# Kernel tuning notes

Measured on AMD Instinct MI355X. Metric: run time of the kernel, lower is better.

The kernel has to match this reference:

```python
import jax, jax.numpy as jnp
import numpy as np

EPS_LN = 1e-5


def fwht(x):
    """Fast Walsh-Hadamard transform over the last axis (power-of-two length).
    Vectorized butterfly: log2(n) stages, each a reshape + add/sub."""
    orig_shape = x.shape
    n = orig_shape[-1]
    y = x.reshape(-1, n)
    h = 1
    while h < n:
        y = y.reshape(-1, n // (2 * h), 2, h)
        a = y[:, :, 0, :]
        b = y[:, :, 1, :]
        y = jnp.stack([a + b, a - b], axis=2).reshape(-1, n)
        h <<= 1
    return y.reshape(orig_shape)


def setup_inputs() -> dict:
    key = jax.random.key(0)
    kx, kw, kg = jax.random.split(key, 3)
    B, S, D_IN, D_OUT = 4, 4096, 2048, 2048
    x = jax.random.normal(kx, (B, S, D_IN), dtype=jnp.float32)
    # kaiming_uniform_(a=sqrt(5)) -> bound = 1/sqrt(in_features)
    bound = 1.0 / np.sqrt(D_IN)
    W = jax.random.uniform(kw, (D_OUT, D_IN), dtype=jnp.float32,
                           minval=-bound, maxval=bound)
    gamma = jnp.ones((D_IN,), dtype=jnp.float32)
    beta = jnp.zeros((D_IN,), dtype=jnp.float32)
    return {"x": x, "W": W, "gamma": gamma, "beta": beta}


def reference(x, W, gamma, beta):
    bits = 4
    max_val = (1 << (bits - 1)) - 1  # 7
    # LayerNorm over last dim
    mu = jnp.mean(x, axis=-1, keepdims=True)
    var = jnp.mean(jnp.square(x - mu), axis=-1, keepdims=True)
    x_ln = (x - mu) * jax.lax.rsqrt(var + EPS_LN) * gamma + beta
    # Activation fake-quant to `bits` bits (per-row absmax scale)
    x_scale = jnp.clip(jnp.max(jnp.abs(x_ln), axis=-1, keepdims=True), 1e-6, None)
    x_int = jnp.clip(jnp.round(x_ln * max_val / x_scale), -max_val, max_val)
    x_q = x_int * x_scale / max_val
    # Hadamard transform of quantized activations
    x_h = fwht(x_q)
    # Ternary weight quantization with global mean-abs scale
    w_scale = jnp.clip(jnp.mean(jnp.abs(W)), 1e-6, None)
    w_q = (jnp.where(W > 0.5 * w_scale, 1.0, 0.0)
           + jnp.where(W < -0.5 * w_scale, -1.0, 0.0)) * w_scale
    # Linear (no bias), then second Hadamard transform
    out = jnp.einsum('bsd,od->bso', x_h, w_q)
    return fwht(out)
```

## Files before the change

kernel.cpp:

```cpp
#include <hip/hip_runtime.h>

typedef unsigned short u16;
typedef __attribute__((ext_vector_type(8))) __bf16 bf16x8;
typedef __attribute__((ext_vector_type(4))) float floatx4;

#define DDIM 2048
#define MROWS 16384

__device__ __forceinline__ u16 f2bf(float f) {
    unsigned int u = __builtin_bit_cast(unsigned int, f);
    u = (u + 0x7fffu + ((u >> 16) & 1u)) >> 16;
    return (u16)u;
}

__device__ __forceinline__ float wave_sum(float v) {
#pragma unroll
    for (int o = 32; o > 0; o >>= 1) v += __shfl_down(v, o, 64);
    return v;
}
__device__ __forceinline__ float wave_max(float v) {
#pragma unroll
    for (int o = 32; o > 0; o >>= 1) v = fmaxf(v, __shfl_down(v, o, 64));
    return v;
}

__global__ __launch_bounds__(256) void absmean_part(const float4* __restrict__ W4,
                                                    float* __restrict__ partial) {
    float s = 0.f;
    for (int i = blockIdx.x * 256 + threadIdx.x; i < (DDIM * DDIM / 4); i += 1024 * 256) {
        float4 v = W4[i];
        s += fabsf(v.x) + fabsf(v.y) + fabsf(v.z) + fabsf(v.w);
    }
    s = wave_sum(s);
    __shared__ float red[4];
    if ((threadIdx.x & 63) == 0) red[threadIdx.x >> 6] = s;
    __syncthreads();
    if (threadIdx.x == 0) partial[blockIdx.x] = red[0] + red[1] + red[2] + red[3];
}

#define CFP 9

template <bool QUANT, bool BF16OUT>
__global__ __launch_bounds__(256) void colfwht(const float* __restrict__ in,
                                               void* __restrict__ out,
                                               const float* __restrict__ partial) {
    extern __shared__ float S[];
    const int t = threadIdx.x;
    const int c8 = blockIdx.x * 8;

    float wsc = 0.f, half_t = 0.f;
    if (QUANT) {
        __shared__ float wred[4];
        float s = partial[t] + partial[t + 256] + partial[t + 512] + partial[t + 768];
        s = wave_sum(s);
        if ((t & 63) == 0) wred[t >> 6] = s;
        __syncthreads();
        float m = (wred[0] + wred[1] + wred[2] + wred[3]) * (1.0f / (float)(DDIM * DDIM));
        wsc = fmaxf(m, 1e-6f);
        half_t = 0.5f * wsc;
    }

#pragma unroll
    for (int i = 0; i < 16; ++i) {
        const int k = i * 256 + t;
        const int row = k >> 1, half = k & 1;
        float4 v = *(const float4*)(in + (size_t)row * DDIM + c8 + half * 4);
        if (QUANT) {
            v.x = (v.x > half_t ? wsc : 0.f) + (v.x < -half_t ? -wsc : 0.f);
            v.y = (v.y > half_t ? wsc : 0.f) + (v.y < -half_t ? -wsc : 0.f);
            v.z = (v.z > half_t ? wsc : 0.f) + (v.z < -half_t ? -wsc : 0.f);
            v.w = (v.w > half_t ? wsc : 0.f) + (v.w < -half_t ? -wsc : 0.f);
        }
        float* sp = S + row * CFP + half * 4;
        sp[0] = v.x; sp[1] = v.y; sp[2] = v.z; sp[3] = v.w;
    }
    __syncthreads();

#pragma unroll
    for (int s = 0; s < 5; ++s) {
        const int h = 1 << (2 * s);
#pragma unroll
        for (int i = 0; i < 16; ++i) {
            const int task = i * 256 + t;
            const int p = task >> 3, c = task & 7;
            const int i0 = ((p >> (2 * s)) << (2 * s + 2)) | (p & (h - 1));
            float* a0 = S + (size_t)i0 * CFP + c;
            const float x0 = a0[0];
            const float x1 = a0[(size_t)h * CFP];
            const float x2 = a0[(size_t)2 * h * CFP];
            const float x3 = a0[(size_t)3 * h * CFP];
            const float s01 = x0 + x1, d01 = x0 - x1;
            const float s23 = x2 + x3, d23 = x2 - x3;
            a0[0]                   = s01 + s23;
            a0[(size_t)h * CFP]     = d01 + d23;
            a0[(size_t)2 * h * CFP] = s01 - s23;
            a0[(size_t)3 * h * CFP] = d01 - d23;
        }
        __syncthreads();
    }
#pragma unroll
    for (int i = 0; i < 32; ++i) {
        const int task = i * 256 + t;
        const int p = task >> 3, c = task & 7;
        float* a0 = S + (size_t)p * CFP + c;
        const float x0 = a0[0];
        const float x1 = a0[(size_t)1024 * CFP];
        a0[0] = x0 + x1;
        a0[(size_t)1024 * CFP] = x0 - x1;
    }
    __syncthreads();

    const int c = t >> 5, l = t & 31;
#pragma unroll
    for (int i = 0; i < 16; ++i) {
        const int o4 = i * 32 + l;
        const float r0 = S[(size_t)(o4 * 4 + 0) * CFP + c];
        const float r1 = S[(size_t)(o4 * 4 + 1) * CFP + c];
        const float r2 = S[(size_t)(o4 * 4 + 2) * CFP + c];
        const float r3 = S[(size_t)(o4 * 4 + 3) * CFP + c];
        if (BF16OUT) {
            uint2 v;
            v.x = (unsigned)f2bf(r0) | ((unsigned)f2bf(r1) << 16);
            v.y = (unsigned)f2bf(r2) | ((unsigned)f2bf(r3) << 16);
            ((uint2*)((u16*)out + (size_t)(c8 + c) * DDIM))[o4] = v;
        } else {
            ((float4*)((float*)out + (size_t)(c8 + c) * DDIM))[o4] =
                make_float4(r0, r1, r2, r3);
        }
    }
}

__global__ __launch_bounds__(256) void ln_quant(const float* __restrict__ X,
                                                const float* __restrict__ G,
                                                const float* __restrict__ Bt,
                                                u16* __restrict__ XQ) {
    const int row = blockIdx.x;
    const int t = threadIdx.x;
    const float4* rp = (const float4*)(X + (size_t)row * DDIM);
    float4 v0 = rp[t], v1 = rp[t + 256];
    float v[8] = {v0.x, v0.y, v0.z, v0.w, v1.x, v1.y, v1.z, v1.w};

    __shared__ float redA[4], redB[4], redC[4];
    const int wv = t >> 6, ln = t & 63;

    float s = 0.f, s2 = 0.f;
#pragma unroll
    for (int j = 0; j < 8; ++j) { s += v[j]; s2 += v[j] * v[j]; }
#pragma unroll
    for (int o = 32; o > 0; o >>= 1) {
        s += __shfl_down(s, o, 64);
        s2 += __shfl_down(s2, o, 64);
    }
    if (ln == 0) { redA[wv] = s; redB[wv] = s2; }
    __syncthreads();
    const float mu = (redA[0] + redA[1] + redA[2] + redA[3]) * (1.f / (float)DDIM);
    const float ex2 = (redB[0] + redB[1] + redB[2] + redB[3]) * (1.f / (float)DDIM);
    const float var = ex2 - mu * mu;
    const float rstd = rsqrtf(var + 1e-5f);

    const float4* gp = (const float4*)G;
    const float4* bp = (const float4*)Bt;
    float4 g0 = gp[t], g1 = gp[t + 256];
    float4 b0 = bp[t], b1 = bp[t + 256];
    float gg[8] = {g0.x, g0.y, g0.z, g0.w, g1.x, g1.y, g1.z, g1.w};
    float bb[8] = {b0.x, b0.y, b0.z, b0.w, b1.x, b1.y, b1.z, b1.w};

    float y[8];
    float am = 0.f;
#pragma unroll
    for (int j = 0; j < 8; ++j) {
        y[j] = (v[j] - mu) * rstd * gg[j] + bb[j];
        am = fmaxf(am, fabsf(y[j]));
    }
    float w = wave_max(am);
    if (ln == 0) redC[wv] = w;
    __syncthreads();
    const float scale = fmaxf(fmaxf(fmaxf(redC[0], redC[1]), fmaxf(redC[2], redC[3])), 1e-6f);

    const float r7 = 7.f / scale, s7 = scale / 7.f;
    unsigned int q[4];
#pragma unroll
    for (int j = 0; j < 8; j += 2) {
        float qa = fminf(fmaxf(rintf(y[j] * r7), -7.f), 7.f);
        float qb = fminf(fmaxf(rintf(y[j + 1] * r7), -7.f), 7.f);
        q[j >> 1] = (unsigned)f2bf(qa * s7) | ((unsigned)f2bf(qb * s7) << 16);
    }
    uint2 o0, o1;
    o0.x = q[0]; o0.y = q[1]; o1.x = q[2]; o1.y = q[3];
    uint2* orow = (uint2*)(XQ + (size_t)row * DDIM);
    orow[t] = o0;
    orow[t + 256] = o1;
}

#define GBK 64
#define GNT (DDIM / GBK)
#define NITER (GNT / 2)
#define TILEU (256 * GBK)

__device__ __forceinline__ void gl_lds16(const u16* g, u16* l) {
    __builtin_amdgcn_global_load_lds((const __attribute__((address_space(1))) void*)g,
                                     (__attribute__((address_space(3))) void*)l,
                                     16, 0, 0);
}

#define PBAR do {                                                              \
    __builtin_amdgcn_sched_barrier(0);                                         \
    asm volatile("" ::: "memory");                                             \
    __builtin_amdgcn_s_barrier();                                              \
    asm volatile("" ::: "memory");                                             \
    __builtin_amdgcn_sched_barrier(0);                                         \
} while (0)

#define PWAIT8 do {                                                            \
    __builtin_amdgcn_sched_barrier(0);                                         \
    asm volatile("s_waitcnt vmcnt(8)" ::: "memory");                           \
    __builtin_amdgcn_s_barrier();                                              \
    asm volatile("" ::: "memory");                                             \
    __builtin_amdgcn_sched_barrier(0);                                         \
} while (0)

#define PWAIT0 do {                                                            \
    __builtin_amdgcn_sched_barrier(0);                                         \
    asm volatile("s_waitcnt vmcnt(0)" ::: "memory");                           \
    __builtin_amdgcn_s_barrier();                                              \
    asm volatile("" ::: "memory");                                             \
    __builtin_amdgcn_sched_barrier(0);                                         \
} while (0)

__global__ __launch_bounds__(512, 2) void gemm256(const u16* __restrict__ A,
                                                  const u16* __restrict__ B,
                                                  float* __restrict__ C) {
    extern __shared__ __align__(16) u16 lds[];
    const int t = threadIdx.x;
    const int lane = t & 63;
    const int wid = t >> 6;
    const int wm = wid >> 2;
    const int wn = wid & 3;

    const int d = blockIdx.x;
    const int bm = (d & 7) | ((d >> 6) << 3);
    const int bn = (d >> 3) & 7;

    const int l15 = lane & 15;
    const int kq = lane >> 4;
    const int x7 = lane & 7;
    const int c0 = (kq ^ x7) << 3;
    const int c1 = ((kq | 4) ^ x7) << 3;
    const int arow = (wm << 7) + l15;
    const int brow = (wn << 6) + l15;

    const int srow = t >> 3;
    const int gch = ((t & 7) ^ (srow & 7)) << 3;
    const u16* Ag = A + (size_t)(bm * 256 + srow) * DDIM + gch;
    const u16* Bg = B + (size_t)(bn * 256 + srow) * DDIM + gch;
    u16* const AL0 = lds + t * 8;
    u16* const BL0 = lds + TILEU + t * 8;
    u16* const AL1 = lds + 2 * TILEU + t * 8;
    u16* const BL1 = lds + 3 * TILEU + t * 8;
    const u16* const Ab0 = lds;
    const u16* const Bb0 = lds + TILEU;
    const u16* const Ab1 = lds + 2 * TILEU;
    const u16* const Bb1 = lds + 3 * TILEU;

    floatx4 acc[8][4];
#pragma unroll
    for (int i = 0; i < 8; ++i)
#pragma unroll
        for (int j = 0; j < 4; ++j)
#pragma unroll
            for (int e = 0; e < 4; ++e) acc[i][j][e] = 0.f;

    bf16x8 a[4][2], b0v[2][2], b1v[2][2];

#define STGA(dst, q, ko) gl_lds16(Ag + (size_t)((q) * 64) * DDIM + (ko), (dst) + (q) * 4096)
#define STGB(dst, q, ko) gl_lds16(Bg + (size_t)((q) * 64) * DDIM + (ko), (dst) + (q) * 4096)

#define LDA(Ab, mh)                                                            \
    _Pragma("unroll") for (int fm = 0; fm < 4; ++fm) {                         \
        const u16* p = (Ab) + (arow + (mh) * 64 + fm * 16) * GBK;              \
        a[fm][0] = *(const bf16x8*)(p + c0);                                   \
        a[fm][1] = *(const bf16x8*)(p + c1);                                   \
    }

#define LDB(dst, Bb, nh)                                                       \
    _Pragma("unroll") for (int fn = 0; fn < 2; ++fn) {                         \
        const u16* p = (Bb) + (brow + (nh) * 32 + fn * 16) * GBK;              \
        dst[fn][0] = *(const bf16x8*)(p + c0);                                 \
        dst[fn][1] = *(const bf16x8*)(p + c1);                                 \
    }

#define MMA(mh, bsrc, nh)                                                      \
    __builtin_amdgcn_s_setprio(1);                                             \
    _Pragma("unroll") for (int fm = 0; fm < 4; ++fm)                           \
        _Pragma("unroll") for (int fn = 0; fn < 2; ++fn)                       \
            _Pragma("unroll") for (int ks = 0; ks < 2; ++ks)                   \
                acc[(mh) * 4 + fm][(nh) * 2 + fn] =                            \
                    __builtin_amdgcn_mfma_f32_16x16x32_bf16(                   \
                        a[fm][ks], bsrc[fn][ks],                               \
                        acc[(mh) * 4 + fm][(nh) * 2 + fn], 0, 0, 0);           \
    __builtin_amdgcn_s_setprio(0);

#pragma unroll
    for (int q = 0; q < 4; ++q) STGA(AL0, q, 0);
#pragma unroll
    for (int q = 0; q < 4; ++q) STGB(BL0, q, 0);
#pragma unroll
    for (int q = 0; q < 4; ++q) STGA(AL1, q, GBK);
#pragma unroll
    for (int q = 0; q < 4; ++q) STGB(BL1, q, GBK);
    PWAIT8;

    for (int it = 0; it < NITER; ++it) {
        const int kp0 = (it * 2 + 2) * GBK;
        const int kp1 = kp0 + GBK;
        const bool pf = (it < NITER - 1);

        LDA(Ab0, 0);
        LDB(b0v, Bb0, 0);
        PBAR;
        MMA(0, b0v, 0);
        LDB(b1v, Bb0, 1);
        if (pf) { STGA(AL0, 0, kp0); STGA(AL0, 2, kp0); }
        PBAR;
        MMA(0, b1v, 1);
        LDA(Ab0, 1);
        if (pf) { STGB(BL0, 0, kp0); STGB(BL0, 1, kp0); }
        PBAR;
        MMA(1, b0v, 0);
        if (pf) { STGB(BL0, 2, kp0); STGB(BL0, 3, kp0); STGA(AL0, 1, kp0); STGA(AL0, 3, kp0); }
        if (pf) { PWAIT8; } else { PWAIT0; }
        MMA(1, b1v, 1);

        LDA(Ab1, 0);
        LDB(b0v, Bb1, 0);
        PBAR;
        MMA(0, b0v, 0);
        LDB(b1v, Bb1, 1);
        if (pf) { STGA(AL1, 0, kp1); STGA(AL1, 2, kp1); }
        PBAR;
        MMA(0, b1v, 1);
        LDA(Ab1, 1);
        if (pf) { STGB(BL1, 0, kp1); STGB(BL1, 1, kp1); }
        PBAR;
        MMA(1, b0v, 0);
        if (pf) { STGB(BL1, 2, kp1); STGB(BL1, 3, kp1); STGA(AL1, 1, kp1); STGA(AL1, 3, kp1); }
        if (pf) { PWAIT8; } else { PWAIT0; }
        MMA(1, b1v, 1);
    }

#undef STGA
#undef STGB
#undef LDA
#undef LDB
#undef MMA

    float* Cb = C + (size_t)(bm * 256 + (wm << 7) + (lane >> 4) * 4) * DDIM
                  + bn * 256 + (wn << 6) + l15;
#pragma unroll
    for (int fm = 0; fm < 8; ++fm)
#pragma unroll
        for (int fn = 0; fn < 4; ++fn)
#pragma unroll
            for (int r = 0; r < 4; ++r)
                Cb[(size_t)(fm * 16 + r) * DDIM + fn * 16] = acc[fm][fn][r];
}

extern "C" void kernel_launch(void* const* d_in, const int* in_sizes, int n_in,
                              void* d_out, int out_size, void* d_ws, size_t ws_size,
                              hipStream_t stream) {
    const float* X  = (const float*)d_in[0];
    const float* W  = (const float*)d_in[1];
    const float* G  = (const float*)d_in[2];
    const float* Bt = (const float*)d_in[3];
    float* out = (float*)d_out;

    char* ws = (char*)d_ws;
    u16*   xq   = (u16*)ws;
    float* bufA = (float*)(ws + (size_t)67108864);
    float* bufB = (float*)(ws + (size_t)67108864 + 16777216);
    float* partial = bufB;
    u16*   w3      = (u16*)bufB;

    absmean_part<<<1024, 256, 0, stream>>>((const float4*)W, partial);

    {
        void (*k1)(const float*, void*, const float*) = colfwht<true, false>;
        void (*k2)(const float*, void*, const float*) = colfwht<false, true>;
        hipFuncSetAttribute(reinterpret_cast<const void*>(k1),
                            hipFuncAttributeMaxDynamicSharedMemorySize, DDIM * CFP * 4);
        hipFuncSetAttribute(reinterpret_cast<const void*>(k2),
                            hipFuncAttributeMaxDynamicSharedMemorySize, DDIM * CFP * 4);
        colfwht<true, false><<<256, 256, DDIM * CFP * 4, stream>>>(W, (void*)bufA, partial);
        colfwht<false, true><<<256, 256, DDIM * CFP * 4, stream>>>(bufA, (void*)w3, nullptr);
    }

    ln_quant<<<MROWS, 256, 0, stream>>>(X, G, Bt, xq);

    hipFuncSetAttribute(reinterpret_cast<const void*>(gemm256),
                        hipFuncAttributeMaxDynamicSharedMemorySize, 131072);
    gemm256<<<dim3(512), 512, 131072, stream>>>(xq, w3, out);
}
```

Measured before the change: 386.9 us.

## Fuse weight column-FWHT passes with LayerNorm quantization into shared launches

```diff
diff --git a/kernel.cpp b/kernel.cpp
--- a/kernel.cpp
+++ b/kernel.cpp
@@ -41,28 +41,29 @@
 #define CFP 9
 
 template <bool QUANT, bool BF16OUT>
-__global__ __launch_bounds__(256) void colfwht(const float* __restrict__ in,
-                                               void* __restrict__ out,
-                                               const float* __restrict__ partial) {
-    extern __shared__ float S[];
+__device__ __forceinline__ void colfwht512(const float* __restrict__ in,
+                                           void* __restrict__ out,
+                                           const float* __restrict__ partial,
+                                           int blk, float* S) {
     const int t = threadIdx.x;
-    const int c8 = blockIdx.x * 8;
+    const int c8 = blk * 8;
 
     float wsc = 0.f, half_t = 0.f;
     if (QUANT) {
-        __shared__ float wred[4];
-        float s = partial[t] + partial[t + 256] + partial[t + 512] + partial[t + 768];
+        __shared__ float wred[8];
+        float s = partial[t] + partial[t + 512];
         s = wave_sum(s);
         if ((t & 63) == 0) wred[t >> 6] = s;
         __syncthreads();
-        float m = (wred[0] + wred[1] + wred[2] + wred[3]) * (1.0f / (float)(DDIM * DDIM));
+        float m = (wred[0] + wred[1] + wred[2] + wred[3] +
+                   wred[4] + wred[5] + wred[6] + wred[7]) * (1.0f / (float)(DDIM * DDIM));
         wsc = fmaxf(m, 1e-6f);
         half_t = 0.5f * wsc;
     }
 
 #pragma unroll
-    for (int i = 0; i < 16; ++i) {
-        const int k = i * 256 + t;
+    for (int i = 0; i < 8; ++i) {
+        const int k = i * 512 + t;
         const int row = k >> 1, half = k & 1;
         float4 v = *(const float4*)(in + (size_t)row * DDIM + c8 + half * 4);
         if (QUANT) {
@@ -80,8 +81,8 @@
     for (int s = 0; s < 5; ++s) {
         const int h = 1 << (2 * s);
 #pragma unroll
-        for (int i = 0; i < 16; ++i) {
-            const int task = i * 256 + t;
+        for (int i = 0; i < 8; ++i) {
+            const int task = i * 512 + t;
             const int p = task >> 3, c = task & 7;
             const int i0 = ((p >> (2 * s)) << (2 * s + 2)) | (p & (h - 1));
             float* a0 = S + (size_t)i0 * CFP + c;
@@ -99,8 +100,8 @@
         __syncthreads();
     }
 #pragma unroll
-    for (int i = 0; i < 32; ++i) {
-        const int task = i * 256 + t;
+    for (int i = 0; i < 16; ++i) {
+        const int task = i * 512 + t;
         const int p = task >> 3, c = task & 7;
         float* a0 = S + (size_t)p * CFP + c;
         const float x0 = a0[0];
@@ -110,10 +111,10 @@
     }
     __syncthreads();
 
-    const int c = t >> 5, l = t & 31;
-#pragma unroll
-    for (int i = 0; i < 16; ++i) {
-        const int o4 = i * 32 + l;
+    const int c = t >> 6, l = t & 63;
+#pragma unroll
+    for (int i = 0; i < 8; ++i) {
+        const int o4 = i * 64 + l;
         const float r0 = S[(size_t)(o4 * 4 + 0) * CFP + c];
         const float r1 = S[(size_t)(o4 * 4 + 1) * CFP + c];
         const float r2 = S[(size_t)(o4 * 4 + 2) * CFP + c];
@@ -130,18 +131,20 @@
     }
 }
 
-__global__ __launch_bounds__(256) void ln_quant(const float* __restrict__ X,
-                                                const float* __restrict__ G,
-                                                const float* __restrict__ Bt,
-                                                u16* __restrict__ XQ) {
-    const int row = blockIdx.x;
+__device__ __forceinline__ void ln2_block(const float* __restrict__ X,
+                                          const float* __restrict__ G,
+                                          const float* __restrict__ Bt,
+                                          u16* __restrict__ XQ, int row0) {
     const int t = threadIdx.x;
+    const int half = t >> 8, u = t & 255;
+    const int row = row0 + half;
     const float4* rp = (const float4*)(X + (size_t)row * DDIM);
-    float4 v0 = rp[t], v1 = rp[t + 256];
+    float4 v0 = rp[u], v1 = rp[u + 256];
     float v[8] = {v0.x, v0.y, v0.z, v0.w, v1.x, v1.y, v1.z, v1.w};
 
-    __shared__ float redA[4], redB[4], redC[4];
+    __shared__ float redA[8], redB[8], redC[8];
     const int wv = t >> 6, ln = t & 63;
+    const int b4 = half << 2;
 
     float s = 0.f, s2 = 0.f;
 #pragma unroll
@@ -153,15 +156,15 @@
     }
     if (ln == 0) { redA[wv] = s; redB[wv] = s2; }
     __syncthreads();
-    const float mu = (redA[0] + redA[1] + redA[2] + redA[3]) * (1.f / (float)DDIM);
-    const float ex2 = (redB[0] + redB[1] + redB[2] + redB[3]) * (1.f / (float)DDIM);
+    const float mu = (redA[b4] + redA[b4 + 1] + redA[b4 + 2] + redA[b4 + 3]) * (1.f / (float)DDIM);
+    const float ex2 = (redB[b4] + redB[b4 + 1] + redB[b4 + 2] + redB[b4 + 3]) * (1.f / (float)DDIM);
     const float var = ex2 - mu * mu;
     const float rstd = rsqrtf(var + 1e-5f);
 
     const float4* gp = (const float4*)G;
     const float4* bp = (const float4*)Bt;
-    float4 g0 = gp[t], g1 = gp[t + 256];
-    float4 b0 = bp[t], b1 = bp[t + 256];
+    float4 g0 = gp[u], g1 = gp[u + 256];
+    float4 b0 = bp[u], b1 = bp[u + 256];
     float gg[8] = {g0.x, g0.y, g0.z, g0.w, g1.x, g1.y, g1.z, g1.w};
     float bb[8] = {b0.x, b0.y, b0.z, b0.w, b1.x, b1.y, b1.z, b1.w};
 
@@ -175,7 +178,8 @@
     float w = wave_max(am);
     if (ln == 0) redC[wv] = w;
     __syncthreads();
-    const float scale = fmaxf(fmaxf(fmaxf(redC[0], redC[1]), fmaxf(redC[2], redC[3])), 1e-6f);
+    const float scale = fmaxf(fmaxf(fmaxf(redC[b4], redC[b4 + 1]),
+                                    fmaxf(redC[b4 + 2], redC[b4 + 3])), 1e-6f);
 
     const float r7 = 7.f / scale, s7 = scale / 7.f;
     unsigned int q[4];
@@ -188,8 +192,25 @@
     uint2 o0, o1;
     o0.x = q[0]; o0.y = q[1]; o1.x = q[2]; o1.y = q[3];
     uint2* orow = (uint2*)(XQ + (size_t)row * DDIM);
-    orow[t] = o0;
-    orow[t + 256] = o1;
+    orow[u] = o0;
+    orow[u + 256] = o1;
+}
+
+template <bool QUANT, bool BF16OUT>
+__global__ __launch_bounds__(512) void prep_fused(const float* __restrict__ win,
+                                                  void* __restrict__ wout,
+                                                  const float* __restrict__ partial,
+                                                  const float* __restrict__ X,
+                                                  const float* __restrict__ G,
+                                                  const float* __restrict__ Bt,
+                                                  u16* __restrict__ XQ,
+                                                  int rowbase) {
+    extern __shared__ float S[];
+    if (blockIdx.x < 256) {
+        colfwht512<QUANT, BF16OUT>(win, wout, partial, blockIdx.x, S);
+    } else {
+        ln2_block(X, G, Bt, XQ, rowbase + (int)(blockIdx.x - 256) * 2);
+    }
 }
 
 #define GBK 64
@@ -381,20 +402,24 @@
     float* partial = bufB;
     u16*   w3      = (u16*)bufB;
 
+    const int LDSZ = DDIM * CFP * 4;
+
     absmean_part<<<1024, 256, 0, stream>>>((const float4*)W, partial);
 
     {
-        void (*k1)(const float*, void*, const float*) = colfwht<true, false>;
-        void (*k2)(const float*, void*, const float*) = colfwht<false, true>;
+        void (*k1)(const float*, void*, const float*, const float*, const float*,
+                   const float*, u16*, int) = prep_fused<true, false>;
+        void (*k2)(const float*, void*, const float*, const float*, const float*,
+                   const float*, u16*, int) = prep_fused<false, true>;
         hipFuncSetAttribute(reinterpret_cast<const void*>(k1),
-                            hipFuncAttributeMaxDynamicSharedMemorySize, DDIM * CFP * 4);
+                            hipFuncAttributeMaxDynamicSharedMemorySize, LDSZ);
         hipFuncSetAttribute(reinterpret_cast<const void*>(k2),
-                            hipFuncAttributeMaxDynamicSharedMemorySize, DDIM * CFP * 4);
-        colfwht<true, false><<<256, 256, DDIM * CFP * 4, stream>>>(W, (void*)bufA, partial);
-        colfwht<false, true><<<256, 256, DDIM * CFP * 4, stream>>>(bufA, (void*)w3, nullptr);
-    }
-
-    ln_quant<<<MROWS, 256, 0, stream>>>(X, G, Bt, xq);
+                            hipFuncAttributeMaxDynamicSharedMemorySize, LDSZ);
+        prep_fused<true, false><<<256 + 4096, 512, LDSZ, stream>>>(
+            W, (void*)bufA, partial, X, G, Bt, xq, 0);
+        prep_fused<false, true><<<256 + 4096, 512, LDSZ, stream>>>(
+            bufA, (void*)w3, nullptr, X, G, Bt, xq, 8192);
+    }
 
     hipFuncSetAttribute(reinterpret_cast<const void*>(gemm256),
                         hipFuncAttributeMaxDynamicSharedMemorySize, 131072);
```

New measurement: 374.9 us. 3.1% less time.
